# Kernel optimization log

Measured on AMD Instinct MI355X. Metric: run time of the kernel, lower is better.

The kernel has to match this reference:

```python
import jax, jax.numpy as jnp
import numpy as np

H = 1536          # hidden_size
NUM_HEADS = 12
NUM_KV = 2
HEAD_DIM = 128
GQA_REP = NUM_HEADS // NUM_KV  # 6
MAX_CACHE = 131072
SCALE = HEAD_DIM ** -0.5


def setup_inputs() -> dict:
    key = jax.random.key(0)
    ks = jax.random.split(key, 8)
    w = 0.02  # weight init scale for numerical sanity
    return {
        "hidden_states": jax.random.normal(ks[0], (1, H, 1, 1), dtype=jnp.float32),
        "Wq": jax.random.normal(ks[1], (NUM_HEADS * HEAD_DIM, H), dtype=jnp.float32) * w,
        "Wk": jax.random.normal(ks[2], (NUM_KV * HEAD_DIM, H), dtype=jnp.float32) * w,
        "Wv": jax.random.normal(ks[3], (NUM_KV * HEAD_DIM, H), dtype=jnp.float32) * w,
        "Wo": jax.random.normal(ks[4], (H, NUM_HEADS * HEAD_DIM), dtype=jnp.float32) * w,
        "kv_cache_k": jax.random.normal(ks[5], (1, NUM_KV, MAX_CACHE, HEAD_DIM), dtype=jnp.float32),
        "kv_cache_v": jax.random.normal(ks[6], (1, NUM_KV, MAX_CACHE, HEAD_DIM), dtype=jnp.float32),
        "pos": MAX_CACHE - 1,  # python int: current cache write position
    }


def reference(hidden_states, Wq, Wk, Wv, Wo, kv_cache_k, kv_cache_v, pos):
    # 1x1 Conv2d on a [1,H,1,1] tensor == matvec.
    x = hidden_states.reshape(H)                      # [H]
    q = (Wq @ x).reshape(NUM_KV, GQA_REP, HEAD_DIM)   # [g, r, d]
    k = (Wk @ x).reshape(NUM_KV, 1, HEAD_DIM)         # [g, 1, d]
    v = (Wv @ x).reshape(NUM_KV, 1, HEAD_DIM)
    # in-place cache write at pos (pos < MAX_CACHE in this setup)
    kc = jax.lax.dynamic_update_slice(kv_cache_k[0], k, (0, pos, 0))  # [g, L, d]
    vc = jax.lax.dynamic_update_slice(kv_cache_v[0], v, (0, pos, 0))
    seq_len = min(pos + 1, MAX_CACHE)  # pos is a python int -> static slice
    kc = kc[:, :seq_len, :]
    vc = vc[:, :seq_len, :]
    # GQA without materializing repeated K/V: fold repeat into the q head axis.
    scores = jnp.einsum('grd,gld->grl', q, kc) * SCALE       # [g, r, L]
    attn = jax.nn.softmax(scores, axis=-1)
    out = jnp.einsum('grl,gld->grd', attn, vc)               # [g, r, d]
    y = Wo @ out.reshape(NUM_HEADS * HEAD_DIM)               # [H]
    return y.reshape(1, H, 1, 1)
```

## Files before the change

kernel.cpp:

```cpp
#include <hip/hip_runtime.h>
#include <math.h>

#define HDIM 1536
#define NUM_HEADS 12
#define NUM_KV 2
#define HEAD_DIM 128
#define GQA_REP 6
#define MAX_CACHE 131072
#define SCALE 0.08838834764831845f
#define FIXED_MAX 8.0f

#define WS_Q    0
#define WS_OUT  2048
#define WS_L2   4096
#define WS_PART 65536
#define REC 132

#define NEG_BIG (-1.0e30f)
#define MASK_NEG (-1.0e38f)

__global__ __launch_bounds__(256) void proj_qkv(
    const float* __restrict__ x, const float* __restrict__ Wq,
    const float* __restrict__ Wk, const float* __restrict__ Wv,
    float* __restrict__ kv_k, float* __restrict__ kv_v,
    const int* __restrict__ pos_p, float* __restrict__ ws)
{
    int r    = (blockIdx.x * 256 + threadIdx.x) >> 6;
    int lane = threadIdx.x & 63;

    const float* Wrow;
    if (r < HDIM)            Wrow = Wq + (size_t)r * HDIM;
    else if (r < HDIM + 256) Wrow = Wk + (size_t)(r - HDIM) * HDIM;
    else                     Wrow = Wv + (size_t)(r - HDIM - 256) * HDIM;

    const float4* w4 = (const float4*)Wrow;
    const float4* x4 = (const float4*)x;
    float sum = 0.f;
#pragma unroll
    for (int it = 0; it < 6; ++it) {
        float4 a = w4[lane + 64 * it];
        float4 b = x4[lane + 64 * it];
        sum += a.x * b.x + a.y * b.y + a.z * b.z + a.w * b.w;
    }
#pragma unroll
    for (int off = 32; off >= 1; off >>= 1) sum += __shfl_xor(sum, off);

    if (lane == 0) {
        if (r < HDIM) {
            ws[WS_Q + r] = sum * SCALE;
        } else {
            int pos = *pos_p;
            if (r < HDIM + 256) {
                int j = r - HDIM; int g = j >> 7, d = j & 127;
                kv_k[((size_t)g * MAX_CACHE + pos) * HEAD_DIM + d] = sum;
            } else {
                int j = r - HDIM - 256; int g = j >> 7, d = j & 127;
                kv_v[((size_t)g * MAX_CACHE + pos) * HEAD_DIM + d] = sum;
            }
        }
    }
}

__device__ inline float xgrp_sum(float v) {
    v += __shfl_xor(v, 16);
    v += __shfl_xor(v, 32);
    return v;
}

__global__ __launch_bounds__(256) void attn_decode(
    const float* __restrict__ kv_k, const float* __restrict__ kv_v,
    const int* __restrict__ pos_p, float* __restrict__ ws)
{
    int wv   = (blockIdx.x * 256 + threadIdx.x) >> 6;
    int lane = threadIdx.x & 63;
    int g   = wv >> 10;
    int u   = wv & 1023;
    int grp = lane >> 4;
    int j   = lane & 15;

    int seq_len = *pos_p + 1;
    if (seq_len > MAX_CACHE) seq_len = MAX_CACHE;

    const float* qb = ws + WS_Q + g * (GQA_REP * HEAD_DIM);
    float4 q0[GQA_REP], q1[GQA_REP];
#pragma unroll
    for (int r = 0; r < GQA_REP; ++r) {
        const float4* qr = (const float4*)(qb + r * HEAD_DIM);
        q0[r] = qr[j];
        q1[r] = qr[j + 16];
    }

    float  l[GQA_REP];
    float4 a0[GQA_REP], a1[GQA_REP];
#pragma unroll
    for (int r = 0; r < GQA_REP; ++r) {
        l[r] = 0.f;
        a0[r].x = a0[r].y = a0[r].z = a0[r].w = 0.f;
        a1[r].x = a1[r].y = a1[r].z = a1[r].w = 0.f;
    }

    int base = u * 128;
    const float4* Kb = (const float4*)(kv_k + ((size_t)g * MAX_CACHE + base) * HEAD_DIM);
    const float4* Vb = (const float4*)(kv_v + ((size_t)g * MAX_CACHE + base) * HEAD_DIM);
    int idx0 = grp * 32 + j;

    float4 K0 = Kb[idx0], K1 = Kb[idx0 + 16];
    float4 V0 = Vb[idx0], V1 = Vb[idx0 + 16];

    for (int i = 0; i < 32; ++i) {
        float4 K0n, K1n, V0n, V1n;
        if (i < 31) {
            int o = idx0 + (i + 1) * 128;
            K0n = Kb[o];  K1n = Kb[o + 16];
            V0n = Vb[o];  V1n = Vb[o + 16];
        }
        int p = base + i * 4 + grp;
        float maskadd = (p < seq_len) ? 0.f : MASK_NEG;

#pragma unroll
        for (int r = 0; r < GQA_REP; ++r) {
            float s = K0.x * q0[r].x + K0.y * q0[r].y + K0.z * q0[r].z + K0.w * q0[r].w
                    + K1.x * q1[r].x + K1.y * q1[r].y + K1.z * q1[r].z + K1.w * q1[r].w;
#pragma unroll
            for (int off = 8; off >= 1; off >>= 1) s += __shfl_xor(s, off);
            float pw = __expf(s + maskadd - FIXED_MAX);
            l[r] += pw;
            a0[r].x += pw * V0.x; a0[r].y += pw * V0.y;
            a0[r].z += pw * V0.z; a0[r].w += pw * V0.w;
            a1[r].x += pw * V1.x; a1[r].y += pw * V1.y;
            a1[r].z += pw * V1.z; a1[r].w += pw * V1.w;
        }
        K0 = K0n; K1 = K1n; V0 = V0n; V1 = V1n;
    }

#pragma unroll
    for (int r = 0; r < GQA_REP; ++r) {
        l[r] = xgrp_sum(l[r]);
        a0[r].x = xgrp_sum(a0[r].x); a0[r].y = xgrp_sum(a0[r].y);
        a0[r].z = xgrp_sum(a0[r].z); a0[r].w = xgrp_sum(a0[r].w);
        a1[r].x = xgrp_sum(a1[r].x); a1[r].y = xgrp_sum(a1[r].y);
        a1[r].z = xgrp_sum(a1[r].z); a1[r].w = xgrp_sum(a1[r].w);

        float* rec = ws + WS_PART + ((size_t)(g * 1024 + u) * GQA_REP + r) * REC;
        if (lane < 16) {
            ((float4*)(rec + 4))[j]      = a0[r];
            ((float4*)(rec + 4))[j + 16] = a1[r];
        }
        if (lane == 0) rec[0] = l[r];
    }
}

__global__ __launch_bounds__(64) void combine1(float* __restrict__ ws)
{
    int b  = blockIdx.x;
    int hh = b >> 5;
    int s  = b & 31;
    int g = hh / GQA_REP, r = hh % GQA_REP;
    int t  = threadIdx.x;

    const float* base = ws + WS_PART +
        ((size_t)(g * 1024 + s * 32) * GQA_REP + r) * REC;
    const size_t stride = (size_t)GQA_REP * REC;

    float lu = (t < 32) ? base[(size_t)t * stride] : 0.f;
#pragma unroll
    for (int off = 32; off >= 1; off >>= 1) lu += __shfl_xor(lu, off);

    float2 a; a.x = 0.f; a.y = 0.f;
    for (int uu = 0; uu < 32; ++uu) {
        float2 av = ((const float2*)(base + (size_t)uu * stride + 4))[t];
        a.x += av.x;
        a.y += av.y;
    }
    float* orec = ws + WS_L2 + (size_t)(hh * 32 + s) * REC;
    ((float2*)(orec + 4))[t] = a;
    if (t == 0) orec[0] = lu;
}

__global__ __launch_bounds__(64) void combine2(float* __restrict__ ws)
{
    int hh = blockIdx.x;
    int t  = threadIdx.x;

    const float* base = ws + WS_L2 + (size_t)(hh * 32) * REC;

    float lu = (t < 32) ? base[(size_t)t * REC] : 0.f;
#pragma unroll
    for (int off = 32; off >= 1; off >>= 1) lu += __shfl_xor(lu, off);

    float2 a; a.x = 0.f; a.y = 0.f;
    for (int uu = 0; uu < 32; ++uu) {
        float2 av = ((const float2*)(base + (size_t)uu * REC + 4))[t];
        a.x += av.x;
        a.y += av.y;
    }
    float invL = 1.f / lu;
    ws[WS_OUT + hh * HEAD_DIM + 2 * t]     = a.x * invL;
    ws[WS_OUT + hh * HEAD_DIM + 2 * t + 1] = a.y * invL;
}

__global__ __launch_bounds__(256) void proj_out(
    const float* __restrict__ Wo, const float* __restrict__ ws,
    float* __restrict__ y)
{
    int r    = (blockIdx.x * 256 + threadIdx.x) >> 6;
    int lane = threadIdx.x & 63;
    const float4* w4 = (const float4*)(Wo + (size_t)r * HDIM);
    const float4* o4 = (const float4*)(ws + WS_OUT);
    float sum = 0.f;
#pragma unroll
    for (int it = 0; it < 6; ++it) {
        float4 a = w4[lane + 64 * it];
        float4 b = o4[lane + 64 * it];
        sum += a.x * b.x + a.y * b.y + a.z * b.z + a.w * b.w;
    }
#pragma unroll
    for (int off = 32; off >= 1; off >>= 1) sum += __shfl_xor(sum, off);
    if (lane == 0) y[r] = sum;
}

extern "C" void kernel_launch(void* const* d_in, const int* in_sizes, int n_in,
                              void* d_out, int out_size, void* d_ws, size_t ws_size,
                              hipStream_t stream) {
    const float* x   = (const float*)d_in[0];
    const float* Wq  = (const float*)d_in[1];
    const float* Wk  = (const float*)d_in[2];
    const float* Wv  = (const float*)d_in[3];
    const float* Wo  = (const float*)d_in[4];
    float*       kvk = (float*)d_in[5];
    float*       kvv = (float*)d_in[6];
    const int*   pos = (const int*)d_in[7];
    float* ws = (float*)d_ws;
    float* y  = (float*)d_out;

    proj_qkv   <<<512, 256, 0, stream>>>(x, Wq, Wk, Wv, kvk, kvv, pos, ws);
    attn_decode<<<512, 256, 0, stream>>>(kvk, kvv, pos, ws);
    combine1   <<<384,  64, 0, stream>>>(ws);
    combine2   <<< 12,  64, 0, stream>>>(ws);
    proj_out   <<<384, 256, 0, stream>>>(Wo, ws, y);
}
```

Measured before the change: 316.8 us.

## Fuse decode stages into one cooperative kernel with grid syncs and deeper prefetch

Merges the five separate kernels (QKV projection, attention, two combine stages, output projection) into one cooperative kernel that uses grid-wide syncs between phases, which removes per-launch overhead and inter-kernel gaps. If the cooperative launch fails, the original multi-kernel path runs instead. The attention loop now keeps four K/V rows in flight in registers rather than one, to hide more memory latency. Grid syncs cost something per phase, and 512 blocks with launch bounds of two blocks per CU must all be co-resident. The extra register arrays could also lower occupancy.

```diff
diff --git a/kernel.cpp b/kernel.cpp
--- a/kernel.cpp
+++ b/kernel.cpp
@@ -1,5 +1,8 @@
 #include <hip/hip_runtime.h>
+#include <hip/hip_cooperative_groups.h>
 #include <math.h>
+
+namespace cg = cooperative_groups;
 
 #define HDIM 1536
 #define NUM_HEADS 12
@@ -16,18 +19,16 @@
 #define WS_PART 65536
 #define REC 132
 
-#define NEG_BIG (-1.0e30f)
 #define MASK_NEG (-1.0e38f)
 
-__global__ __launch_bounds__(256) void proj_qkv(
+__device__ __forceinline__ void phase_proj_qkv(
+    int gw, int lane,
     const float* __restrict__ x, const float* __restrict__ Wq,
     const float* __restrict__ Wk, const float* __restrict__ Wv,
     float* __restrict__ kv_k, float* __restrict__ kv_v,
     const int* __restrict__ pos_p, float* __restrict__ ws)
 {
-    int r    = (blockIdx.x * 256 + threadIdx.x) >> 6;
-    int lane = threadIdx.x & 63;
-
+    int r = gw;
     const float* Wrow;
     if (r < HDIM)            Wrow = Wq + (size_t)r * HDIM;
     else if (r < HDIM + 256) Wrow = Wk + (size_t)(r - HDIM) * HDIM;
@@ -51,30 +52,29 @@
         } else {
             int pos = *pos_p;
             if (r < HDIM + 256) {
-                int j = r - HDIM; int g = j >> 7, d = j & 127;
+                int jj = r - HDIM; int g = jj >> 7, d = jj & 127;
                 kv_k[((size_t)g * MAX_CACHE + pos) * HEAD_DIM + d] = sum;
             } else {
-                int j = r - HDIM - 256; int g = j >> 7, d = j & 127;
+                int jj = r - HDIM - 256; int g = jj >> 7, d = jj & 127;
                 kv_v[((size_t)g * MAX_CACHE + pos) * HEAD_DIM + d] = sum;
             }
         }
     }
 }
 
-__device__ inline float xgrp_sum(float v) {
+__device__ __forceinline__ float xgrp_sum(float v) {
     v += __shfl_xor(v, 16);
     v += __shfl_xor(v, 32);
     return v;
 }
 
-__global__ __launch_bounds__(256) void attn_decode(
+__device__ __forceinline__ void phase_attn(
+    int gw, int lane,
     const float* __restrict__ kv_k, const float* __restrict__ kv_v,
     const int* __restrict__ pos_p, float* __restrict__ ws)
 {
-    int wv   = (blockIdx.x * 256 + threadIdx.x) >> 6;
-    int lane = threadIdx.x & 63;
-    int g   = wv >> 10;
-    int u   = wv & 1023;
+    int g   = gw >> 10;
+    int u   = gw & 1023;
     int grp = lane >> 4;
     int j   = lane & 15;
 
@@ -104,33 +104,41 @@
     const float4* Vb = (const float4*)(kv_v + ((size_t)g * MAX_CACHE + base) * HEAD_DIM);
     int idx0 = grp * 32 + j;
 
-    float4 K0 = Kb[idx0], K1 = Kb[idx0 + 16];
-    float4 V0 = Vb[idx0], V1 = Vb[idx0 + 16];
-
-    for (int i = 0; i < 32; ++i) {
-        float4 K0n, K1n, V0n, V1n;
-        if (i < 31) {
-            int o = idx0 + (i + 1) * 128;
-            K0n = Kb[o];  K1n = Kb[o + 16];
-            V0n = Vb[o];  V1n = Vb[o + 16];
+    float4 K0[4], K1[4], V0[4], V1[4];
+#pragma unroll
+    for (int b = 0; b < 4; ++b) {
+        int o = idx0 + b * 128;
+        K0[b] = Kb[o];      K1[b] = Kb[o + 16];
+        V0[b] = Vb[o];      V1[b] = Vb[o + 16];
+    }
+
+    for (int i = 0; i < 32; i += 4) {
+#pragma unroll
+        for (int b = 0; b < 4; ++b) {
+            int ii = i + b;
+            int p = base + ii * 4 + grp;
+            float maskadd = (p < seq_len) ? 0.f : MASK_NEG;
+
+#pragma unroll
+            for (int r = 0; r < GQA_REP; ++r) {
+                float s = K0[b].x * q0[r].x + K0[b].y * q0[r].y
+                        + K0[b].z * q0[r].z + K0[b].w * q0[r].w
+                        + K1[b].x * q1[r].x + K1[b].y * q1[r].y
+                        + K1[b].z * q1[r].z + K1[b].w * q1[r].w;
+#pragma unroll
+                for (int off = 8; off >= 1; off >>= 1) s += __shfl_xor(s, off);
+                float pw = __expf(s + maskadd - FIXED_MAX);
+                l[r] += pw;
+                a0[r].x += pw * V0[b].x; a0[r].y += pw * V0[b].y;
+                a0[r].z += pw * V0[b].z; a0[r].w += pw * V0[b].w;
+                a1[r].x += pw * V1[b].x; a1[r].y += pw * V1[b].y;
+                a1[r].z += pw * V1[b].z; a1[r].w += pw * V1[b].w;
+            }
+            int nx = ii + 4;
+            int o = (nx < 32) ? (idx0 + nx * 128) : idx0;
+            K0[b] = Kb[o];      K1[b] = Kb[o + 16];
+            V0[b] = Vb[o];      V1[b] = Vb[o + 16];
         }
-        int p = base + i * 4 + grp;
-        float maskadd = (p < seq_len) ? 0.f : MASK_NEG;
-
-#pragma unroll
-        for (int r = 0; r < GQA_REP; ++r) {
-            float s = K0.x * q0[r].x + K0.y * q0[r].y + K0.z * q0[r].z + K0.w * q0[r].w
-                    + K1.x * q1[r].x + K1.y * q1[r].y + K1.z * q1[r].z + K1.w * q1[r].w;
-#pragma unroll
-            for (int off = 8; off >= 1; off >>= 1) s += __shfl_xor(s, off);
-            float pw = __expf(s + maskadd - FIXED_MAX);
-            l[r] += pw;
-            a0[r].x += pw * V0.x; a0[r].y += pw * V0.y;
-            a0[r].z += pw * V0.z; a0[r].w += pw * V0.w;
-            a1[r].x += pw * V1.x; a1[r].y += pw * V1.y;
-            a1[r].z += pw * V1.z; a1[r].w += pw * V1.w;
-        }
-        K0 = K0n; K1 = K1n; V0 = V0n; V1 = V1n;
     }
 
 #pragma unroll
@@ -150,13 +158,11 @@
     }
 }
 
-__global__ __launch_bounds__(64) void combine1(float* __restrict__ ws)
-{
-    int b  = blockIdx.x;
+__device__ __forceinline__ void phase_combine1(int b, int t, float* __restrict__ ws)
+{
     int hh = b >> 5;
     int s  = b & 31;
     int g = hh / GQA_REP, r = hh % GQA_REP;
-    int t  = threadIdx.x;
 
     const float* base = ws + WS_PART +
         ((size_t)(g * 1024 + s * 32) * GQA_REP + r) * REC;
@@ -177,11 +183,8 @@
     if (t == 0) orec[0] = lu;
 }
 
-__global__ __launch_bounds__(64) void combine2(float* __restrict__ ws)
-{
-    int hh = blockIdx.x;
-    int t  = threadIdx.x;
-
+__device__ __forceinline__ void phase_combine2(int hh, int t, float* __restrict__ ws)
+{
     const float* base = ws + WS_L2 + (size_t)(hh * 32) * REC;
 
     float lu = (t < 32) ? base[(size_t)t * REC] : 0.f;
@@ -199,12 +202,11 @@
     ws[WS_OUT + hh * HEAD_DIM + 2 * t + 1] = a.y * invL;
 }
 
-__global__ __launch_bounds__(256) void proj_out(
+__device__ __forceinline__ void phase_proj_out(
+    int r, int lane,
     const float* __restrict__ Wo, const float* __restrict__ ws,
     float* __restrict__ y)
 {
-    int r    = (blockIdx.x * 256 + threadIdx.x) >> 6;
-    int lane = threadIdx.x & 63;
     const float4* w4 = (const float4*)(Wo + (size_t)r * HDIM);
     const float4* o4 = (const float4*)(ws + WS_OUT);
     float sum = 0.f;
@@ -217,6 +219,69 @@
 #pragma unroll
     for (int off = 32; off >= 1; off >>= 1) sum += __shfl_xor(sum, off);
     if (lane == 0) y[r] = sum;
+}
+
+__global__ __launch_bounds__(256, 2) void fused_decode(
+    const float* __restrict__ x, const float* __restrict__ Wq,
+    const float* __restrict__ Wk, const float* __restrict__ Wv,
+    const float* __restrict__ Wo,
+    float* __restrict__ kv_k, float* __restrict__ kv_v,
+    const int* __restrict__ pos_p, float* __restrict__ ws,
+    float* __restrict__ y)
+{
+    cg::grid_group grid = cg::this_grid();
+    int gw   = (blockIdx.x * 256 + (int)threadIdx.x) >> 6;
+    int lane = threadIdx.x & 63;
+
+    phase_proj_qkv(gw, lane, x, Wq, Wk, Wv, kv_k, kv_v, pos_p, ws);
+    grid.sync();
+
+    phase_attn(gw, lane, kv_k, kv_v, pos_p, ws);
+    grid.sync();
+
+    if (gw < 384) phase_combine1(gw, lane, ws);
+    grid.sync();
+
+    if (gw < 12) phase_combine2(gw, lane, ws);
+    grid.sync();
+
+    if (gw < 1536) phase_proj_out(gw, lane, Wo, ws, y);
+}
+
+__global__ __launch_bounds__(256) void k_proj_qkv(
+    const float* __restrict__ x, const float* __restrict__ Wq,
+    const float* __restrict__ Wk, const float* __restrict__ Wv,
+    float* __restrict__ kv_k, float* __restrict__ kv_v,
+    const int* __restrict__ pos_p, float* __restrict__ ws)
+{
+    int gw = (blockIdx.x * 256 + (int)threadIdx.x) >> 6;
+    phase_proj_qkv(gw, threadIdx.x & 63, x, Wq, Wk, Wv, kv_k, kv_v, pos_p, ws);
+}
+
+__global__ __launch_bounds__(256, 2) void k_attn(
+    const float* __restrict__ kv_k, const float* __restrict__ kv_v,
+    const int* __restrict__ pos_p, float* __restrict__ ws)
+{
+    int gw = (blockIdx.x * 256 + (int)threadIdx.x) >> 6;
+    phase_attn(gw, threadIdx.x & 63, kv_k, kv_v, pos_p, ws);
+}
+
+__global__ __launch_bounds__(64) void k_combine1(float* __restrict__ ws)
+{
+    phase_combine1(blockIdx.x, threadIdx.x, ws);
+}
+
+__global__ __launch_bounds__(64) void k_combine2(float* __restrict__ ws)
+{
+    phase_combine2(blockIdx.x, threadIdx.x, ws);
+}
+
+__global__ __launch_bounds__(256) void k_proj_out(
+    const float* __restrict__ Wo, const float* __restrict__ ws,
+    float* __restrict__ y)
+{
+    int gw = (blockIdx.x * 256 + (int)threadIdx.x) >> 6;
+    phase_proj_out(gw, threadIdx.x & 63, Wo, ws, y);
 }
 
 extern "C" void kernel_launch(void* const* d_in, const int* in_sizes, int n_in,
@@ -233,9 +298,15 @@
     float* ws = (float*)d_ws;
     float* y  = (float*)d_out;
 
-    proj_qkv   <<<512, 256, 0, stream>>>(x, Wq, Wk, Wv, kvk, kvv, pos, ws);
-    attn_decode<<<512, 256, 0, stream>>>(kvk, kvv, pos, ws);
-    combine1   <<<384,  64, 0, stream>>>(ws);
-    combine2   <<< 12,  64, 0, stream>>>(ws);
-    proj_out   <<<384, 256, 0, stream>>>(Wo, ws, y);
-}
+    void* args[] = { (void*)&x, (void*)&Wq, (void*)&Wk, (void*)&Wv, (void*)&Wo,
+                     (void*)&kvk, (void*)&kvv, (void*)&pos, (void*)&ws, (void*)&y };
+    hipError_t e = hipLaunchCooperativeKernel((void*)fused_decode,
+                                              dim3(512), dim3(256), args, 0, stream);
+    if (e != hipSuccess) {
+        k_proj_qkv <<<512, 256, 0, stream>>>(x, Wq, Wk, Wv, kvk, kvv, pos, ws);
+        k_attn     <<<512, 256, 0, stream>>>(kvk, kvv, pos, ws);
+        k_combine1 <<<384,  64, 0, stream>>>(ws);
+        k_combine2 <<< 12,  64, 0, stream>>>(ws);
+        k_proj_out <<<384, 256, 0, stream>>>(Wo, ws, y);
+    }
+}
```

Result: slower. 544.3 us (+71.8%).

## Split attention across more waves with half-warp per key and full-chunk fast path

Applied to the files above, without the earlier changes.

The attention kernel now maps 32 lanes per key position (one float4 each) instead of 16 lanes with two float4s, so each wave handles two positions per step. The split count doubles to 2048 waves per KV group when the workspace is large enough, and the combine kernels are templated to match. A mask-free path runs for chunks that lie fully inside seq_len, and launch bounds request higher occupancy. The aim is more memory-level parallelism on the KV cache stream, at the cost of a larger partial-record buffer and a deeper shuffle reduction per score.

```diff
diff --git a/kernel.cpp b/kernel.cpp
--- a/kernel.cpp
+++ b/kernel.cpp
@@ -13,10 +13,8 @@
 #define WS_Q    0
 #define WS_OUT  2048
 #define WS_L2   4096
-#define WS_PART 65536
 #define REC 132
 
-#define NEG_BIG (-1.0e30f)
 #define MASK_NEG (-1.0e38f)
 
 __global__ __launch_bounds__(256) void proj_qkv(
@@ -25,7 +23,7 @@
     float* __restrict__ kv_k, float* __restrict__ kv_v,
     const int* __restrict__ pos_p, float* __restrict__ ws)
 {
-    int r    = (blockIdx.x * 256 + threadIdx.x) >> 6;
+    int r    = (blockIdx.x * 256 + (int)threadIdx.x) >> 6;
     int lane = threadIdx.x & 63;
 
     const float* Wrow;
@@ -51,115 +49,126 @@
         } else {
             int pos = *pos_p;
             if (r < HDIM + 256) {
-                int j = r - HDIM; int g = j >> 7, d = j & 127;
+                int jj = r - HDIM; int g = jj >> 7, d = jj & 127;
                 kv_k[((size_t)g * MAX_CACHE + pos) * HEAD_DIM + d] = sum;
             } else {
-                int j = r - HDIM - 256; int g = j >> 7, d = j & 127;
+                int jj = r - HDIM - 256; int g = jj >> 7, d = jj & 127;
                 kv_v[((size_t)g * MAX_CACHE + pos) * HEAD_DIM + d] = sum;
             }
         }
     }
 }
 
-__device__ inline float xgrp_sum(float v) {
-    v += __shfl_xor(v, 16);
-    v += __shfl_xor(v, 32);
-    return v;
-}
-
-__global__ __launch_bounds__(256) void attn_decode(
+__device__ __forceinline__ void attn_step(
+    const float4 K, const float4 V, float maskbias,
+    const float4 q[GQA_REP], float l[GQA_REP], float4 acc[GQA_REP])
+{
+#pragma unroll
+    for (int r = 0; r < GQA_REP; ++r) {
+        float s = K.x * q[r].x + K.y * q[r].y + K.z * q[r].z + K.w * q[r].w;
+#pragma unroll
+        for (int off = 16; off >= 1; off >>= 1) s += __shfl_xor(s, off);
+        float pw = __expf(s + maskbias);
+        l[r] += pw;
+        acc[r].x += pw * V.x;
+        acc[r].y += pw * V.y;
+        acc[r].z += pw * V.z;
+        acc[r].w += pw * V.w;
+    }
+}
+
+template<int UPG, int WSPART>
+__global__ __launch_bounds__(256, 4) void k_attn(
     const float* __restrict__ kv_k, const float* __restrict__ kv_v,
     const int* __restrict__ pos_p, float* __restrict__ ws)
 {
-    int wv   = (blockIdx.x * 256 + threadIdx.x) >> 6;
+    constexpr int POS_PER = MAX_CACHE / UPG;
+    constexpr int ITER    = POS_PER / 2;
+
+    int wv   = (blockIdx.x * 256 + (int)threadIdx.x) >> 6;
     int lane = threadIdx.x & 63;
-    int g   = wv >> 10;
-    int u   = wv & 1023;
-    int grp = lane >> 4;
-    int j   = lane & 15;
+    int g = wv / UPG;
+    int u = wv & (UPG - 1);
+    int h = lane >> 5;
+    int j = lane & 31;
 
     int seq_len = *pos_p + 1;
     if (seq_len > MAX_CACHE) seq_len = MAX_CACHE;
 
     const float* qb = ws + WS_Q + g * (GQA_REP * HEAD_DIM);
-    float4 q0[GQA_REP], q1[GQA_REP];
-#pragma unroll
-    for (int r = 0; r < GQA_REP; ++r) {
-        const float4* qr = (const float4*)(qb + r * HEAD_DIM);
-        q0[r] = qr[j];
-        q1[r] = qr[j + 16];
-    }
+    float4 q[GQA_REP];
+#pragma unroll
+    for (int r = 0; r < GQA_REP; ++r)
+        q[r] = ((const float4*)(qb + r * HEAD_DIM))[j];
 
     float  l[GQA_REP];
-    float4 a0[GQA_REP], a1[GQA_REP];
+    float4 acc[GQA_REP];
 #pragma unroll
     for (int r = 0; r < GQA_REP; ++r) {
         l[r] = 0.f;
-        a0[r].x = a0[r].y = a0[r].z = a0[r].w = 0.f;
-        a1[r].x = a1[r].y = a1[r].z = a1[r].w = 0.f;
-    }
-
-    int base = u * 128;
+        acc[r].x = acc[r].y = acc[r].z = acc[r].w = 0.f;
+    }
+
+    int base = u * POS_PER;
     const float4* Kb = (const float4*)(kv_k + ((size_t)g * MAX_CACHE + base) * HEAD_DIM);
     const float4* Vb = (const float4*)(kv_v + ((size_t)g * MAX_CACHE + base) * HEAD_DIM);
-    int idx0 = grp * 32 + j;
-
-    float4 K0 = Kb[idx0], K1 = Kb[idx0 + 16];
-    float4 V0 = Vb[idx0], V1 = Vb[idx0 + 16];
-
-    for (int i = 0; i < 32; ++i) {
-        float4 K0n, K1n, V0n, V1n;
-        if (i < 31) {
-            int o = idx0 + (i + 1) * 128;
-            K0n = Kb[o];  K1n = Kb[o + 16];
-            V0n = Vb[o];  V1n = Vb[o + 16];
+    int idx = h * 32 + j;
+
+    bool full = (base + POS_PER) <= seq_len;
+
+    float4 Ka = Kb[idx],      Va = Vb[idx];
+    float4 Kc = Kb[idx + 64], Vc = Vb[idx + 64];
+
+    if (full) {
+        for (int i = 0; i < ITER; i += 2) {
+            int o2 = (i + 2 < ITER) ? idx + (i + 2) * 64 : idx;
+            int o3 = (i + 3 < ITER) ? idx + (i + 3) * 64 : idx;
+            float4 Kp = Kb[o2], Vp = Vb[o2];
+            float4 Kq = Kb[o3], Vq = Vb[o3];
+            attn_step(Ka, Va, -FIXED_MAX, q, l, acc);
+            attn_step(Kc, Vc, -FIXED_MAX, q, l, acc);
+            Ka = Kp; Va = Vp; Kc = Kq; Vc = Vq;
         }
-        int p = base + i * 4 + grp;
-        float maskadd = (p < seq_len) ? 0.f : MASK_NEG;
-
-#pragma unroll
-        for (int r = 0; r < GQA_REP; ++r) {
-            float s = K0.x * q0[r].x + K0.y * q0[r].y + K0.z * q0[r].z + K0.w * q0[r].w
-                    + K1.x * q1[r].x + K1.y * q1[r].y + K1.z * q1[r].z + K1.w * q1[r].w;
-#pragma unroll
-            for (int off = 8; off >= 1; off >>= 1) s += __shfl_xor(s, off);
-            float pw = __expf(s + maskadd - FIXED_MAX);
-            l[r] += pw;
-            a0[r].x += pw * V0.x; a0[r].y += pw * V0.y;
-            a0[r].z += pw * V0.z; a0[r].w += pw * V0.w;
-            a1[r].x += pw * V1.x; a1[r].y += pw * V1.y;
-            a1[r].z += pw * V1.z; a1[r].w += pw * V1.w;
+    } else {
+        for (int i = 0; i < ITER; i += 2) {
+            int o2 = (i + 2 < ITER) ? idx + (i + 2) * 64 : idx;
+            int o3 = (i + 3 < ITER) ? idx + (i + 3) * 64 : idx;
+            float4 Kp = Kb[o2], Vp = Vb[o2];
+            float4 Kq = Kb[o3], Vq = Vb[o3];
+            int p0 = base + 2 * i + h;
+            int p1 = p0 + 2;
+            attn_step(Ka, Va, (p0 < seq_len) ? -FIXED_MAX : MASK_NEG, q, l, acc);
+            attn_step(Kc, Vc, (p1 < seq_len) ? -FIXED_MAX : MASK_NEG, q, l, acc);
+            Ka = Kp; Va = Vp; Kc = Kq; Vc = Vq;
         }
-        K0 = K0n; K1 = K1n; V0 = V0n; V1 = V1n;
     }
 
 #pragma unroll
     for (int r = 0; r < GQA_REP; ++r) {
-        l[r] = xgrp_sum(l[r]);
-        a0[r].x = xgrp_sum(a0[r].x); a0[r].y = xgrp_sum(a0[r].y);
-        a0[r].z = xgrp_sum(a0[r].z); a0[r].w = xgrp_sum(a0[r].w);
-        a1[r].x = xgrp_sum(a1[r].x); a1[r].y = xgrp_sum(a1[r].y);
-        a1[r].z = xgrp_sum(a1[r].z); a1[r].w = xgrp_sum(a1[r].w);
-
-        float* rec = ws + WS_PART + ((size_t)(g * 1024 + u) * GQA_REP + r) * REC;
-        if (lane < 16) {
-            ((float4*)(rec + 4))[j]      = a0[r];
-            ((float4*)(rec + 4))[j + 16] = a1[r];
-        }
+        l[r]     += __shfl_xor(l[r], 32);
+        acc[r].x += __shfl_xor(acc[r].x, 32);
+        acc[r].y += __shfl_xor(acc[r].y, 32);
+        acc[r].z += __shfl_xor(acc[r].z, 32);
+        acc[r].w += __shfl_xor(acc[r].w, 32);
+
+        float* rec = ws + WSPART + ((size_t)(g * UPG + u) * GQA_REP + r) * REC;
+        if (lane < 32) ((float4*)(rec + 4))[j] = acc[r];
         if (lane == 0) rec[0] = l[r];
     }
 }
 
-__global__ __launch_bounds__(64) void combine1(float* __restrict__ ws)
-{
+template<int UPG, int WSPART>
+__global__ __launch_bounds__(64) void k_combine1(float* __restrict__ ws)
+{
+    constexpr int SPH = UPG / 32;
     int b  = blockIdx.x;
-    int hh = b >> 5;
-    int s  = b & 31;
+    int hh = b / SPH;
+    int s  = b & (SPH - 1);
     int g = hh / GQA_REP, r = hh % GQA_REP;
     int t  = threadIdx.x;
 
-    const float* base = ws + WS_PART +
-        ((size_t)(g * 1024 + s * 32) * GQA_REP + r) * REC;
+    const float* base = ws + WSPART +
+        ((size_t)(g * UPG + s * 32) * GQA_REP + r) * REC;
     const size_t stride = (size_t)GQA_REP * REC;
 
     float lu = (t < 32) ? base[(size_t)t * stride] : 0.f;
@@ -167,29 +176,33 @@
     for (int off = 32; off >= 1; off >>= 1) lu += __shfl_xor(lu, off);
 
     float2 a; a.x = 0.f; a.y = 0.f;
+#pragma unroll 4
     for (int uu = 0; uu < 32; ++uu) {
         float2 av = ((const float2*)(base + (size_t)uu * stride + 4))[t];
         a.x += av.x;
         a.y += av.y;
     }
-    float* orec = ws + WS_L2 + (size_t)(hh * 32 + s) * REC;
+    float* orec = ws + WS_L2 + (size_t)(hh * SPH + s) * REC;
     ((float2*)(orec + 4))[t] = a;
     if (t == 0) orec[0] = lu;
 }
 
-__global__ __launch_bounds__(64) void combine2(float* __restrict__ ws)
-{
+template<int UPG>
+__global__ __launch_bounds__(64) void k_combine2(float* __restrict__ ws)
+{
+    constexpr int SPH = UPG / 32;
     int hh = blockIdx.x;
     int t  = threadIdx.x;
 
-    const float* base = ws + WS_L2 + (size_t)(hh * 32) * REC;
-
-    float lu = (t < 32) ? base[(size_t)t * REC] : 0.f;
+    const float* base = ws + WS_L2 + (size_t)(hh * SPH) * REC;
+
+    float lu = (t < SPH) ? base[(size_t)t * REC] : 0.f;
 #pragma unroll
     for (int off = 32; off >= 1; off >>= 1) lu += __shfl_xor(lu, off);
 
     float2 a; a.x = 0.f; a.y = 0.f;
-    for (int uu = 0; uu < 32; ++uu) {
+#pragma unroll 4
+    for (int uu = 0; uu < SPH; ++uu) {
         float2 av = ((const float2*)(base + (size_t)uu * REC + 4))[t];
         a.x += av.x;
         a.y += av.y;
@@ -203,7 +216,7 @@
     const float* __restrict__ Wo, const float* __restrict__ ws,
     float* __restrict__ y)
 {
-    int r    = (blockIdx.x * 256 + threadIdx.x) >> 6;
+    int r    = (blockIdx.x * 256 + (int)threadIdx.x) >> 6;
     int lane = threadIdx.x & 63;
     const float4* w4 = (const float4*)(Wo + (size_t)r * HDIM);
     const float4* o4 = (const float4*)(ws + WS_OUT);
@@ -233,9 +246,18 @@
     float* ws = (float*)d_ws;
     float* y  = (float*)d_out;
 
-    proj_qkv   <<<512, 256, 0, stream>>>(x, Wq, Wk, Wv, kvk, kvv, pos, ws);
-    attn_decode<<<512, 256, 0, stream>>>(kvk, kvv, pos, ws);
-    combine1   <<<384,  64, 0, stream>>>(ws);
-    combine2   <<< 12,  64, 0, stream>>>(ws);
-    proj_out   <<<384, 256, 0, stream>>>(Wo, ws, y);
-}
+    proj_qkv<<<512, 256, 0, stream>>>(x, Wq, Wk, Wv, kvk, kvv, pos, ws);
+
+    const size_t need2048 = (size_t)(131072 + 2 * 2048 * GQA_REP * REC) * 4;
+    if (ws_size >= need2048) {
+        k_attn    <2048, 131072><<<1024, 256, 0, stream>>>(kvk, kvv, pos, ws);
+        k_combine1<2048, 131072><<<12 * 64, 64, 0, stream>>>(ws);
+        k_combine2<2048>        <<<12,      64, 0, stream>>>(ws);
+    } else {
+        k_attn    <1024, 65536><<<512,     256, 0, stream>>>(kvk, kvv, pos, ws);
+        k_combine1<1024, 65536><<<12 * 32,  64, 0, stream>>>(ws);
+        k_combine2<1024>       <<<12,       64, 0, stream>>>(ws);
+    }
+
+    proj_out<<<384, 256, 0, stream>>>(Wo, ws, y);
+}
```

After: 322.5 us. Within noise of the previous version (+1.8%).
